# Optimization experiments

Measured on AMD Instinct MI355X. Metric: run time of the kernel, lower is better.

## Reference

```python
import jax, jax.numpy as jnp
import numpy as np

N, D, NUM_CLASSES = 4096, 1024, 100
CHUNK = 16  # rows per block; block intermediate is CHUNK x N x D (~256 MB fp32)


def setup_inputs() -> dict:
    key = jax.random.key(0)
    k1, k2 = jax.random.split(key)
    feats = jax.random.uniform(k1, (N, D), dtype=jnp.float32)
    labels = jax.random.randint(k2, (N,), 0, NUM_CLASSES)
    image_idxs = jnp.arange(N)
    return {"feats": feats, "labels": labels, "image_idxs": image_idxs,
            "normalize_feats": 1}


def _cheb_dist(feats):
    """All-pairs Chebyshev distance, computed in row blocks to avoid an N x N x D tensor."""
    n, d = feats.shape
    chunks = feats.reshape(n // CHUNK, CHUNK, d)

    def row_block(fc):  # fc: [CHUNK, D] -> [CHUNK, N]
        return jnp.max(jnp.abs(fc[:, None, :] - feats[None, :, :]), axis=2)

    return jax.lax.map(row_block, chunks).reshape(n, n)  # dist[i, j] = max_d |f_i - f_j|


def reference(feats, labels, image_idxs, normalize_feats):
    n = feats.shape[0]
    feats = feats.reshape(n, -1)
    if normalize_feats:
        feats = feats / jnp.max(feats, axis=1, keepdims=True)
    dist = _cheb_dist(feats)                      # symmetric [N, N]
    same_label = labels[:, None] == labels[None, :]
    masked = jnp.where(same_label, jnp.inf, dist)  # mask same-label rows per column
    closest_idx = jnp.argmin(masked, axis=0)       # hardest different-label negative per column
    loss = dist[jnp.arange(n), closest_idx].mean()
    closest_pairs = image_idxs[closest_idx]
    return loss, closest_pairs
```

## Files before the change

kernel.cpp:

```cpp
#include <hip/hip_runtime.h>
#include <hip/hip_bf16.h>
#include <cfloat>

#define NROWS 4096
#define DDIM 1024
#define NT 64
#define NBLK (NT * (NT + 1) / 2)
#define NSLOT (NT + 1)

#define MAX3ABS(ACC, X, Y) (ACC) = fmaxf(fmaxf(fabsf(X), fabsf(Y)), (ACC))

#define MERGE(BV, BI, V, I) \
    do { if ((V) < (BV) || ((V) == (BV) && (I) < (BI))) { BV = (V); BI = (I); } } while (0)

__global__ __launch_bounds__(256) void normalize_kernel(const float* __restrict__ feats,
                                                        const int* __restrict__ normflag,
                                                        float* __restrict__ normf) {
    const int wave = threadIdx.x >> 6;
    const int lane = threadIdx.x & 63;
    const int row  = blockIdx.x * 4 + wave;
    const float* fr = feats + (size_t)row * DDIM;
    float*       fw = normf + (size_t)row * DDIM;
    float4 v[4];
    float m = 0.0f;
#pragma unroll
    for (int k = 0; k < 4; ++k) {
        v[k] = *(const float4*)(fr + lane * 4 + k * 256);
        m = fmaxf(fmaxf(fmaxf(m, v[k].x), fmaxf(v[k].y, v[k].z)), v[k].w);
    }
#pragma unroll
    for (int off = 32; off > 0; off >>= 1) m = fmaxf(m, __shfl_xor(m, off));
    const float r = (*normflag != 0) ? m : 1.0f;
#pragma unroll
    for (int k = 0; k < 4; ++k) {
        v[k].x /= r; v[k].y /= r; v[k].z /= r; v[k].w /= r;
        *(float4*)(fw + lane * 4 + k * 256) = v[k];
    }
}

__global__ __launch_bounds__(256) void rowmax_kernel(const float* __restrict__ feats,
                                                     const int* __restrict__ normflag,
                                                     float* __restrict__ rowmax) {
    const int wave = threadIdx.x >> 6;
    const int lane = threadIdx.x & 63;
    const int row  = blockIdx.x * 4 + wave;
    const float* fr = feats + (size_t)row * DDIM;
    float m = 0.0f;
    for (int d = lane * 4; d < DDIM; d += 256) {
        float4 v = *(const float4*)(fr + d);
        m = fmaxf(fmaxf(fmaxf(m, v.x), fmaxf(v.y, v.z)), v.w);
    }
#pragma unroll
    for (int off = 32; off > 0; off >>= 1) m = fmaxf(m, __shfl_xor(m, off));
    if (lane == 0) rowmax[row] = (*normflag != 0) ? m : 1.0f;
}

template <bool NORM>
__global__ __launch_bounds__(256, 2) void cheb_kernel(const float* __restrict__ src,
                                                      const float* __restrict__ rowmax,
                                                      const int* __restrict__ labels,
                                                      float* __restrict__ pval,
                                                      int* __restrict__ pidx) {
    int bid = blockIdx.x;
    bid = (bid & 7) * (NBLK / 8) + (bid >> 3);
    float fs = sqrtf((float)((2 * NT + 1) * (2 * NT + 1) - 8 * bid));
    int ta = (int)(((float)(2 * NT + 1) - fs) * 0.5f);
    while ((ta + 1) * NT - ((ta + 1) * ta) / 2 <= bid) ++ta;
    while (ta * NT - (ta * (ta - 1)) / 2 > bid) --ta;
    const int tb = ta + (bid - (ta * NT - (ta * (ta - 1)) / 2));
    const int iBase = ta * 64;
    const int jBase = tb * 64;

    const int t    = threadIdx.x;
    const int w    = t >> 6;
    const int lane = t & 63;
    const int ty8  = lane & 7;
    const int tx8  = lane >> 3;

    __shared__ __align__(16) float lds[4096];
    float* As = lds;
    float* Bs = lds + 2048;

    float acc[8][8];
#pragma unroll
    for (int kk = 0; kk < 8; ++kk)
#pragma unroll
        for (int jj = 0; jj < 8; ++jj) acc[kk][jj] = 0.0f;

    const int r0  = t >> 3;
    const int q0  = t & 7;
    const int swz = 4 * (q0 ^ (r0 & 7));
    float* Aw0 = As + r0 * 32 + swz;
    float* Aw1 = As + (r0 + 32) * 32 + swz;
    float* Bw0 = Bs + r0 * 32 + swz;
    float* Bw1 = Bs + (r0 + 32) * 32 + swz;
    const float* gA0 = src + (size_t)(iBase + r0) * DDIM + 4 * q0;
    const float* gA1 = src + (size_t)(iBase + r0 + 32) * DDIM + 4 * q0;
    const float* gB0 = src + (size_t)(jBase + r0) * DDIM + 4 * q0;
    const float* gB1 = src + (size_t)(jBase + r0 + 32) * DDIM + 4 * q0;
    float rA0 = 1.0f, rA1 = 1.0f, rB0 = 1.0f, rB1 = 1.0f;
    if (NORM) {
        rA0 = rowmax[iBase + r0]; rA1 = rowmax[iBase + r0 + 32];
        rB0 = rowmax[jBase + r0]; rB1 = rowmax[jBase + r0 + 32];
    }

    const char* Ab = (const char*)As + ty8 * 128;
    const char* Bb = (const char*)Bs + tx8 * 128;

    float4 pa0 = *(const float4*)(gA0);
    float4 pa1 = *(const float4*)(gA1);
    float4 pb0 = *(const float4*)(gB0);
    float4 pb1 = *(const float4*)(gB1);

    for (int dc = 0; dc < DDIM / 32; ++dc) {
        __syncthreads();
        if (NORM) {
            pa0.x /= rA0; pa0.y /= rA0; pa0.z /= rA0; pa0.w /= rA0;
            pa1.x /= rA1; pa1.y /= rA1; pa1.z /= rA1; pa1.w /= rA1;
            pb0.x /= rB0; pb0.y /= rB0; pb0.z /= rB0; pb0.w /= rB0;
            pb1.x /= rB1; pb1.y /= rB1; pb1.z /= rB1; pb1.w /= rB1;
        }
        *(float4*)Aw0 = pa0;
        *(float4*)Aw1 = pa1;
        *(float4*)Bw0 = pb0;
        *(float4*)Bw1 = pb1;
        __syncthreads();

        if (dc + 1 < DDIM / 32) {
            const int dB = (dc + 1) * 32;
            pa0 = *(const float4*)(gA0 + dB);
            pa1 = *(const float4*)(gA1 + dB);
            pb0 = *(const float4*)(gB0 + dB);
            pb1 = *(const float4*)(gB1 + dB);
        }

#pragma unroll
        for (int qi = 0; qi < 2; ++qi) {
            const int q  = 2 * w + qi;
            const int oa = 16 * (q ^ ty8);
            const int ob = 16 * (q ^ tx8);
            float4 b[8];
#pragma unroll
            for (int jj = 0; jj < 8; ++jj)
                b[jj] = *(const float4*)(Bb + jj * 1024 + ob);
#pragma unroll
            for (int kk = 0; kk < 8; ++kk) {
                const float4 a = *(const float4*)(Ab + kk * 1024 + oa);
#pragma unroll
                for (int jj = 0; jj < 8; ++jj) {
                    const float d0 = a.x - b[jj].x;
                    const float d1 = a.y - b[jj].y;
                    const float d2 = a.z - b[jj].z;
                    const float d3 = a.w - b[jj].w;
                    MAX3ABS(acc[kk][jj], d0, d1);
                    MAX3ABS(acc[kk][jj], d2, d3);
                }
            }
        }
    }

    int lA[8], lB[8];
    if (w == 0) {
#pragma unroll
        for (int kk = 0; kk < 8; ++kk) lA[kk] = labels[iBase + ty8 + 8 * kk];
#pragma unroll
        for (int jj = 0; jj < 8; ++jj) lB[jj] = labels[jBase + tx8 + 8 * jj];
    }

    float* mbuf = lds;
    __syncthreads();
#define WRITE_ACC() do {                                                     \
    _Pragma("unroll")                                                        \
    for (int g = 0; g < 16; ++g) {                                           \
        float4 v;                                                            \
        v.x = acc[g >> 1][(g & 1) * 4 + 0]; v.y = acc[g >> 1][(g & 1) * 4 + 1]; \
        v.z = acc[g >> 1][(g & 1) * 4 + 2]; v.w = acc[g >> 1][(g & 1) * 4 + 3]; \
        *(float4*)(mbuf + lane * 64 + 4 * (g ^ (lane & 15))) = v;            \
    } } while (0)
#define MERGE_ACC() do {                                                     \
    _Pragma("unroll")                                                        \
    for (int g = 0; g < 16; ++g) {                                           \
        float4 v = *(const float4*)(mbuf + lane * 64 + 4 * (g ^ (lane & 15))); \
        acc[g >> 1][(g & 1) * 4 + 0] = fmaxf(acc[g >> 1][(g & 1) * 4 + 0], v.x); \
        acc[g >> 1][(g & 1) * 4 + 1] = fmaxf(acc[g >> 1][(g & 1) * 4 + 1], v.y); \
        acc[g >> 1][(g & 1) * 4 + 2] = fmaxf(acc[g >> 1][(g & 1) * 4 + 2], v.z); \
        acc[g >> 1][(g & 1) * 4 + 3] = fmaxf(acc[g >> 1][(g & 1) * 4 + 3], v.w); \
    } } while (0)
    if (w == 2) WRITE_ACC();
    __syncthreads();
    if (w == 0) MERGE_ACC();
    __syncthreads();
    if (w == 3) WRITE_ACC();
    __syncthreads();
    if (w == 1) { MERGE_ACC(); WRITE_ACC(); }
    __syncthreads();
    if (w == 0) MERGE_ACC();

    if (w == 0) {
#pragma unroll
        for (int jj = 0; jj < 8; ++jj) {
            float bv = FLT_MAX; int bi = 0x7fffffff;
#pragma unroll
            for (int kk = 0; kk < 8; ++kk) {
                const int i = iBase + ty8 + 8 * kk;
                const float v = (lA[kk] == lB[jj]) ? FLT_MAX : acc[kk][jj];
                MERGE(bv, bi, v, i);
            }
#pragma unroll
            for (int off = 1; off <= 4; off <<= 1) {
                const float ov = __shfl_xor(bv, off);
                const int   oi = __shfl_xor(bi, off);
                MERGE(bv, bi, ov, oi);
            }
            if (ty8 == 0) {
                const int j = jBase + tx8 + 8 * jj;
                pval[ta * NROWS + j] = bv;
                pidx[ta * NROWS + j] = bi;
            }
        }
#pragma unroll
        for (int kk = 0; kk < 8; ++kk) {
            float bv = FLT_MAX; int bi = 0x7fffffff;
#pragma unroll
            for (int jj = 0; jj < 8; ++jj) {
                const int j = jBase + tx8 + 8 * jj;
                const float v = (lA[kk] == lB[jj]) ? FLT_MAX : acc[kk][jj];
                MERGE(bv, bi, v, j);
            }
#pragma unroll
            for (int off = 8; off <= 32; off <<= 1) {
                const float ov = __shfl_xor(bv, off);
                const int   oi = __shfl_xor(bi, off);
                MERGE(bv, bi, ov, oi);
            }
            if (tx8 == 0) {
                const int i = iBase + ty8 + 8 * kk;
                pval[(tb + 1) * NROWS + i] = bv;
                pidx[(tb + 1) * NROWS + i] = bi;
            }
        }
    }
}

__global__ __launch_bounds__(256) void finalizeA_kernel(const float* __restrict__ pval,
                                                        const int* __restrict__ pidx,
                                                        const int* __restrict__ image_idxs,
                                                        float* __restrict__ out,
                                                        float* __restrict__ colmin) {
    const int j = blockIdx.x * 256 + threadIdx.x;
    float bv = FLT_MAX; int bi = 0x7fffffff;
    for (int s = 0; s < NSLOT; ++s) {
        const float v = pval[s * NROWS + j];
        const int   i = pidx[s * NROWS + j];
        MERGE(bv, bi, v, i);
    }
    out[1 + j] = (float)image_idxs[bi];
    colmin[j] = bv;
}

__global__ __launch_bounds__(256) void finalizeB_kernel(const float* __restrict__ colmin,
                                                        float* __restrict__ out) {
    const int t = threadIdx.x;
    float s = 0.0f;
#pragma unroll
    for (int k = 0; k < 16; ++k) s += colmin[t + 256 * k];
#pragma unroll
    for (int off = 32; off > 0; off >>= 1) s += __shfl_xor(s, off);
    __shared__ float ss[4];
    if ((t & 63) == 0) ss[t >> 6] = s;
    __syncthreads();
    if (t == 0) out[0] = (ss[0] + ss[1] + ss[2] + ss[3]) / (float)NROWS;
}

extern "C" void kernel_launch(void* const* d_in, const int* in_sizes, int n_in,
                              void* d_out, int out_size, void* d_ws, size_t ws_size,
                              hipStream_t stream) {
    const float* feats      = (const float*)d_in[0];
    const int*   labels     = (const int*)d_in[1];
    const int*   image_idxs = (const int*)d_in[2];
    const int*   normflag   = (const int*)d_in[3];
    float*       out        = (float*)d_out;

    const size_t normBytes = (size_t)NROWS * DDIM * sizeof(float);
    const size_t partBytes = (size_t)NSLOT * NROWS * 8 + NROWS * 4;

    if (ws_size >= normBytes + partBytes) {
        float* normf  = (float*)d_ws;
        float* pval   = (float*)((char*)d_ws + normBytes);
        int*   pidx   = (int*)(pval + NSLOT * NROWS);
        float* colmin = (float*)(pidx + NSLOT * NROWS);
        normalize_kernel<<<NROWS / 4, 256, 0, stream>>>(feats, normflag, normf);
        cheb_kernel<false><<<NBLK, 256, 0, stream>>>(normf, nullptr, labels, pval, pidx);
        finalizeA_kernel<<<NROWS / 256, 256, 0, stream>>>(pval, pidx, image_idxs, out, colmin);
        finalizeB_kernel<<<1, 256, 0, stream>>>(colmin, out);
    } else {
        float* rowmax = (float*)d_ws;
        float* pval   = rowmax + NROWS;
        int*   pidx   = (int*)(pval + NSLOT * NROWS);
        float* colmin = (float*)(pidx + NSLOT * NROWS);
        rowmax_kernel<<<NROWS / 4, 256, 0, stream>>>(feats, normflag, rowmax);
        cheb_kernel<true><<<NBLK, 256, 0, stream>>>(feats, rowmax, labels, pval, pidx);
        finalizeA_kernel<<<NROWS / 256, 256, 0, stream>>>(pval, pidx, image_idxs, out, colmin);
        finalizeB_kernel<<<1, 256, 0, stream>>>(colmin, out);
    }
}
```

Before: 330.8 us.

## Double-buffer LDS tiles with direct global-to-LDS loads in non-normalized path

For the non-normalized template path, tiles are now loaded straight into LDS with the global_load_lds builtin into two ping-pong buffers, so loads of the next chunk overlap compute on the current one without passing through registers. The swizzle is moved into the global address so the read pattern matches the old layout. LDS doubles to 32 KB and launch bounds ask for 3 blocks per CU, which limits registers for the 64-value accumulator and may cause spills. The normalized path keeps the old register-staged scheme, so whether the new code runs depends on which template instance the host launches, likely the pre-normalized buffer.

New measurement: 721.7 us. 2.18x slower.

```diff
diff --git a/kernel.cpp b/kernel.cpp
--- a/kernel.cpp
+++ b/kernel.cpp
@@ -12,6 +12,10 @@
 
 #define MERGE(BV, BI, V, I) \
     do { if ((V) < (BV) || ((V) == (BV) && (I) < (BI))) { BV = (V); BI = (I); } } while (0)
+
+#define GLL16(GP, LP) \
+    __builtin_amdgcn_global_load_lds((const __attribute__((address_space(1))) void*)(GP), \
+                                     (__attribute__((address_space(3))) void*)(LP), 16, 0, 0)
 
 __global__ __launch_bounds__(256) void normalize_kernel(const float* __restrict__ feats,
                                                         const int* __restrict__ normflag,
@@ -56,7 +60,7 @@
 }
 
 template <bool NORM>
-__global__ __launch_bounds__(256, 2) void cheb_kernel(const float* __restrict__ src,
+__global__ __launch_bounds__(256, 3) void cheb_kernel(const float* __restrict__ src,
                                                       const float* __restrict__ rowmax,
                                                       const int* __restrict__ labels,
                                                       float* __restrict__ pval,
@@ -77,9 +81,7 @@
     const int ty8  = lane & 7;
     const int tx8  = lane >> 3;
 
-    __shared__ __align__(16) float lds[4096];
-    float* As = lds;
-    float* Bs = lds + 2048;
+    __shared__ __align__(16) float lds[8192];
 
     float acc[8][8];
 #pragma unroll
@@ -87,75 +89,115 @@
 #pragma unroll
         for (int jj = 0; jj < 8; ++jj) acc[kk][jj] = 0.0f;
 
-    const int r0  = t >> 3;
-    const int q0  = t & 7;
-    const int swz = 4 * (q0 ^ (r0 & 7));
-    float* Aw0 = As + r0 * 32 + swz;
-    float* Aw1 = As + (r0 + 32) * 32 + swz;
-    float* Bw0 = Bs + r0 * 32 + swz;
-    float* Bw1 = Bs + (r0 + 32) * 32 + swz;
-    const float* gA0 = src + (size_t)(iBase + r0) * DDIM + 4 * q0;
-    const float* gA1 = src + (size_t)(iBase + r0 + 32) * DDIM + 4 * q0;
-    const float* gB0 = src + (size_t)(jBase + r0) * DDIM + 4 * q0;
-    const float* gB1 = src + (size_t)(jBase + r0 + 32) * DDIM + 4 * q0;
-    float rA0 = 1.0f, rA1 = 1.0f, rB0 = 1.0f, rB1 = 1.0f;
-    if (NORM) {
-        rA0 = rowmax[iBase + r0]; rA1 = rowmax[iBase + r0 + 32];
-        rB0 = rowmax[jBase + r0]; rB1 = rowmax[jBase + r0 + 32];
-    }
-
-    const char* Ab = (const char*)As + ty8 * 128;
-    const char* Bb = (const char*)Bs + tx8 * 128;
-
-    float4 pa0 = *(const float4*)(gA0);
-    float4 pa1 = *(const float4*)(gA1);
-    float4 pb0 = *(const float4*)(gB0);
-    float4 pb1 = *(const float4*)(gB1);
-
-    for (int dc = 0; dc < DDIM / 32; ++dc) {
+    const char* Ab0 = (const char*)(lds)        + ty8 * 128;
+    const char* Bb0 = (const char*)(lds + 2048) + tx8 * 128;
+    const char* Ab1 = (const char*)(lds + 4096) + ty8 * 128;
+    const char* Bb1 = (const char*)(lds + 6144) + tx8 * 128;
+
+#define COMPUTE(AB, BB) do {                                                  \
+    _Pragma("unroll")                                                         \
+    for (int qi = 0; qi < 2; ++qi) {                                          \
+        const int q  = 2 * w + qi;                                            \
+        const int oa = 16 * (q ^ ty8);                                        \
+        const int ob = 16 * (q ^ tx8);                                        \
+        float4 b[8];                                                          \
+        _Pragma("unroll")                                                     \
+        for (int jj = 0; jj < 8; ++jj)                                        \
+            b[jj] = *(const float4*)((BB) + jj * 1024 + ob);                  \
+        _Pragma("unroll")                                                     \
+        for (int kk = 0; kk < 8; ++kk) {                                      \
+            const float4 a = *(const float4*)((AB) + kk * 1024 + oa);         \
+            _Pragma("unroll")                                                 \
+            for (int jj = 0; jj < 8; ++jj) {                                  \
+                const float d0 = a.x - b[jj].x;                               \
+                const float d1 = a.y - b[jj].y;                               \
+                const float d2 = a.z - b[jj].z;                               \
+                const float d3 = a.w - b[jj].w;                               \
+                MAX3ABS(acc[kk][jj], d0, d1);                                 \
+                MAX3ABS(acc[kk][jj], d2, d3);                                 \
+            }                                                                 \
+        }                                                                     \
+    } } while (0)
+
+    if (!NORM) {
+        const char* gAst[2];
+        const char* gBst[2];
+        char* ldsA0 = (char*)(lds)        + w * 2048;
+        char* ldsB0 = (char*)(lds + 2048) + w * 2048;
+        char* ldsA1 = (char*)(lds + 4096) + w * 2048;
+        char* ldsB1 = (char*)(lds + 6144) + w * 2048;
+#pragma unroll
+        for (int n = 0; n < 2; ++n) {
+            const int s   = w * 128 + n * 64 + lane;
+            const int row = s >> 3;
+            const int c   = s & 7;
+            const int fo  = 4 * (c ^ (row & 7));
+            gAst[n] = (const char*)(src + (size_t)(iBase + row) * DDIM + fo);
+            gBst[n] = (const char*)(src + (size_t)(jBase + row) * DDIM + fo);
+        }
+
+#define STAGE0(DC) do { const int _o = (DC) * 128;                            \
+        GLL16(gAst[0] + _o, ldsA0);        GLL16(gAst[1] + _o, ldsA0 + 1024); \
+        GLL16(gBst[0] + _o, ldsB0);        GLL16(gBst[1] + _o, ldsB0 + 1024); \
+    } while (0)
+#define STAGE1(DC) do { const int _o = (DC) * 128;                            \
+        GLL16(gAst[0] + _o, ldsA1);        GLL16(gAst[1] + _o, ldsA1 + 1024); \
+        GLL16(gBst[0] + _o, ldsB1);        GLL16(gBst[1] + _o, ldsB1 + 1024); \
+    } while (0)
+
+        STAGE0(0);
         __syncthreads();
-        if (NORM) {
+#pragma unroll 1
+        for (int dc = 0; dc < 32; dc += 2) {
+            if (dc + 1 < 32) STAGE1(dc + 1);
+            COMPUTE(Ab0, Bb0);
+            __syncthreads();
+            if (dc + 2 < 32) STAGE0(dc + 2);
+            COMPUTE(Ab1, Bb1);
+            __syncthreads();
+        }
+    } else {
+        float* As = lds;
+        float* Bs = lds + 2048;
+        const int r0  = t >> 3;
+        const int q0  = t & 7;
+        const int swz = 4 * (q0 ^ (r0 & 7));
+        float* Aw0 = As + r0 * 32 + swz;
+        float* Aw1 = As + (r0 + 32) * 32 + swz;
+        float* Bw0 = Bs + r0 * 32 + swz;
+        float* Bw1 = Bs + (r0 + 32) * 32 + swz;
+        const float* gA0 = src + (size_t)(iBase + r0) * DDIM + 4 * q0;
+        const float* gA1 = src + (size_t)(iBase + r0 + 32) * DDIM + 4 * q0;
+        const float* gB0 = src + (size_t)(jBase + r0) * DDIM + 4 * q0;
+        const float* gB1 = src + (size_t)(jBase + r0 + 32) * DDIM + 4 * q0;
+        const float rA0 = rowmax[iBase + r0], rA1 = rowmax[iBase + r0 + 32];
+        const float rB0 = rowmax[jBase + r0], rB1 = rowmax[jBase + r0 + 32];
+
+        float4 pa0 = *(const float4*)(gA0);
+        float4 pa1 = *(const float4*)(gA1);
+        float4 pb0 = *(const float4*)(gB0);
+        float4 pb1 = *(const float4*)(gB1);
+
+#pragma unroll 1
+        for (int dc = 0; dc < DDIM / 32; ++dc) {
+            __syncthreads();
             pa0.x /= rA0; pa0.y /= rA0; pa0.z /= rA0; pa0.w /= rA0;
             pa1.x /= rA1; pa1.y /= rA1; pa1.z /= rA1; pa1.w /= rA1;
             pb0.x /= rB0; pb0.y /= rB0; pb0.z /= rB0; pb0.w /= rB0;
             pb1.x /= rB1; pb1.y /= rB1; pb1.z /= rB1; pb1.w /= rB1;
-        }
-        *(float4*)Aw0 = pa0;
-        *(float4*)Aw1 = pa1;
-        *(float4*)Bw0 = pb0;
-        *(float4*)Bw1 = pb1;
-        __syncthreads();
-
-        if (dc + 1 < DDIM / 32) {
-            const int dB = (dc + 1) * 32;
-            pa0 = *(const float4*)(gA0 + dB);
-            pa1 = *(const float4*)(gA1 + dB);
-            pb0 = *(const float4*)(gB0 + dB);
-            pb1 = *(const float4*)(gB1 + dB);
-        }
-
-#pragma unroll
-        for (int qi = 0; qi < 2; ++qi) {
-            const int q  = 2 * w + qi;
-            const int oa = 16 * (q ^ ty8);
-            const int ob = 16 * (q ^ tx8);
-            float4 b[8];
-#pragma unroll
-            for (int jj = 0; jj < 8; ++jj)
-                b[jj] = *(const float4*)(Bb + jj * 1024 + ob);
-#pragma unroll
-            for (int kk = 0; kk < 8; ++kk) {
-                const float4 a = *(const float4*)(Ab + kk * 1024 + oa);
-#pragma unroll
-                for (int jj = 0; jj < 8; ++jj) {
-                    const float d0 = a.x - b[jj].x;
-                    const float d1 = a.y - b[jj].y;
-                    const float d2 = a.z - b[jj].z;
-                    const float d3 = a.w - b[jj].w;
-                    MAX3ABS(acc[kk][jj], d0, d1);
-                    MAX3ABS(acc[kk][jj], d2, d3);
-                }
-            }
+            *(float4*)Aw0 = pa0;
+            *(float4*)Aw1 = pa1;
+            *(float4*)Bw0 = pb0;
+            *(float4*)Bw1 = pb1;
+            __syncthreads();
+            if (dc + 1 < DDIM / 32) {
+                const int dB = (dc + 1) * 32;
+                pa0 = *(const float4*)(gA0 + dB);
+                pa1 = *(const float4*)(gA1 + dB);
+                pb0 = *(const float4*)(gB0 + dB);
+                pb1 = *(const float4*)(gB1 + dB);
+            }
+            COMPUTE(Ab0, Bb0);
         }
     }
 
```
